# Optimization experiments

Measured on AMD Instinct MI355X. Metric: run time of the kernel, lower is better.

Reference implementation:

```python
import jax, jax.numpy as jnp
import numpy as np

NUM_NODES = 200000
NUM_EDGES = 600000
NUM_GRAPHS = 10000
BN_EPS = 1e-5


def setup_inputs() -> dict:
    key = jax.random.key(0)
    ks = jax.random.split(key, 10)
    x = jax.random.normal(ks[0], (NUM_NODES, 78), dtype=jnp.float32)
    edge_index = jax.random.randint(ks[1], (2, NUM_EDGES), 0, NUM_NODES, dtype=jnp.int64 if jax.config.jax_enable_x64 else jnp.int32)
    batch = jnp.sort(jax.random.randint(ks[2], (NUM_NODES,), 0, NUM_GRAPHS))
    def glorot(k, shape):
        fan_in, fan_out = shape[-2], shape[-1]
        s = jnp.sqrt(2.0 / (fan_in + fan_out))
        return jax.random.normal(k, shape, dtype=jnp.float32) * s
    return {
        "x": x,
        "edge_index": edge_index,
        "batch": batch,
        "W1_0": glorot(ks[3], (78, 128)),
        "b1_0": jnp.zeros((128,), jnp.float32),
        "W2_0": glorot(ks[4], (128, 128)),
        "b2_0": jnp.zeros((128,), jnp.float32),
        "g_0": jnp.ones((128,), jnp.float32),
        "be_0": jnp.zeros((128,), jnp.float32),
        "W1s": glorot(ks[5], (4, 128, 128)),
        "b1s": jnp.zeros((4, 128), jnp.float32),
        "W2s": glorot(ks[6], (4, 128, 128)),
        "b2s": jnp.zeros((4, 128), jnp.float32),
        "gs": jnp.ones((4, 128), jnp.float32),
        "bes": jnp.zeros((4, 128), jnp.float32),
        "fcW": glorot(ks[7], (128, 64)),
        "fcb": jnp.zeros((64,), jnp.float32),
    }


def _batchnorm(h, gamma, beta):
    # BatchNorm1d with batch statistics (training-mode normalization)
    mean = h.mean(axis=0)
    var = h.var(axis=0)  # biased, as torch uses for normalization
    return gamma * (h - mean) * jax.lax.rsqrt(var + BN_EPS) + beta


def _gin_block(h, src, dst, W1, b1, W2, b2, gamma, beta):
    # GINConv (eps=0): MLP(x + sum of neighbor messages), then ReLU + BN
    agg = jax.ops.segment_sum(h[src], dst, num_segments=NUM_NODES)  # [N, d]
    z = h + agg
    z = jax.nn.relu(z @ W1 + b1) @ W2 + b2
    z = jax.nn.relu(z)
    return _batchnorm(z, gamma, beta)


def reference(x, edge_index, batch, W1_0, b1_0, W2_0, b2_0, g_0, be_0,
              W1s, b1s, W2s, b2s, gs, bes, fcW, fcb):
    src, dst = edge_index[0], edge_index[1]
    h = _gin_block(x, src, dst, W1_0, b1_0, W2_0, b2_0, g_0, be_0)  # [N, 128]

    def body(h, params):
        W1, b1, W2, b2, g, be = params
        return _gin_block(h, src, dst, W1, b1, W2, b2, g, be), None

    h, _ = jax.lax.scan(body, h, (W1s, b1s, W2s, b2s, gs, bes))

    pooled = jax.ops.segment_sum(h, batch, num_segments=NUM_GRAPHS)  # [G, 128]
    out = jax.nn.relu(pooled @ fcW + fcb)  # [G, 64]; dropout is identity at eval
    return out
```

## Files before the change

### kernel.cpp

```cpp
#include <hip/hip_runtime.h>
#include <hip/hip_bf16.h>

#define NN 200000
#define NE 600000
#define NG 10000
#define NCH 98

typedef __attribute__((ext_vector_type(8))) short bfrag;
typedef __attribute__((ext_vector_type(4))) float f32x4;
typedef unsigned short u16;

static __device__ __forceinline__ u16 f2b(float x) {
  __hip_bfloat16 b = __float2bfloat16(x);
  return __builtin_bit_cast(u16, b);
}
static __device__ __forceinline__ float b2f(u16 u) {
  __hip_bfloat16 b = __builtin_bit_cast(__hip_bfloat16, u);
  return __bfloat162float(b);
}
static __device__ __forceinline__ void split(float v, u16& hi, u16& lo) {
  hi = f2b(v);
  lo = f2b(v - b2f(hi));
}

__global__ void prep_kernel(const float* __restrict__ W1_0, const float* __restrict__ W2_0,
                            const float* __restrict__ W1s, const float* __restrict__ W2s,
                            u16* __restrict__ wf) {
  int i = blockIdx.x * 256 + threadIdx.x;
  if (i >= 312 * 64) return;
  int t = i >> 6, lane = i & 63;
  const float* W;
  int KS, ct, kk, Krows, base, half;
  if (t < 24) {
    W = W1_0; KS = 3; ct = t / 3; kk = t - ct * 3; Krows = 78; base = 0; half = 12288;
  } else if (t < 56) {
    int u = t - 24;
    W = W2_0; KS = 4; ct = u >> 2; kk = u & 3; Krows = 128; base = 24576; half = 16384;
  } else {
    int u = t - 56;
    int j = u >> 6, r = u & 63;
    KS = 4; Krows = 128; half = 16384;
    if (r < 32) {
      W = W1s + j * 16384; ct = r >> 2; kk = r & 3; base = 57344 + j * 65536;
    } else {
      W = W2s + j * 16384; r -= 32; ct = r >> 2; kk = r & 3; base = 57344 + j * 65536 + 32768;
    }
  }
  int col = ct * 16 + (lane & 15);
  int idx = ((ct * KS + kk) * 64 + lane) * 8;
  for (int jj = 0; jj < 8; jj++) {
    int k = kk * 32 + 8 * (lane >> 4) + jj;
    float v = (k < Krows) ? W[k * 128 + col] : 0.f;
    u16 hi, lo;
    split(v, hi, lo);
    wf[base + idx + jj] = hi;
    wf[base + half + idx + jj] = lo;
  }
}

__global__ void hist_kernel(const int* __restrict__ dst, int* __restrict__ deg) {
  int e = blockIdx.x * 256 + threadIdx.x;
  if (e < NE) atomicAdd(&deg[dst[e]], 1);
}

__global__ void scan1_kernel(const int* __restrict__ deg, int* __restrict__ csum) {
  __shared__ int s[256];
  int base = blockIdx.x * 2048 + threadIdx.x * 8;
  int t = 0;
#pragma unroll
  for (int j = 0; j < 8; j++) {
    int idx = base + j;
    if (idx < NN) t += deg[idx];
  }
  s[threadIdx.x] = t;
  __syncthreads();
  for (int o = 128; o > 0; o >>= 1) {
    if (threadIdx.x < o) s[threadIdx.x] += s[threadIdx.x + o];
    __syncthreads();
  }
  if (threadIdx.x == 0) csum[blockIdx.x] = s[0];
}

__global__ void scan2_kernel(int* __restrict__ csum, int* __restrict__ rowptr) {
  int acc = 0;
  for (int i = 0; i < NCH; i++) {
    int v = csum[i];
    csum[i] = acc;
    acc += v;
  }
  rowptr[NN] = acc;
}

__global__ void scan3_kernel(const int* deg, const int* __restrict__ csum,
                             int* __restrict__ rowptr, int* cursor) {
  __shared__ int s[256];
  int tid = threadIdx.x;
  int base = blockIdx.x * 2048 + tid * 8;
  int loc[8];
  int t = 0;
#pragma unroll
  for (int j = 0; j < 8; j++) {
    int idx = base + j;
    int d = (idx < NN) ? deg[idx] : 0;
    loc[j] = t;
    t += d;
  }
  s[tid] = t;
  __syncthreads();
  for (int o = 1; o < 256; o <<= 1) {
    int u = (tid >= o) ? s[tid - o] : 0;
    __syncthreads();
    s[tid] += u;
    __syncthreads();
  }
  int off = csum[blockIdx.x] + s[tid] - t;
#pragma unroll
  for (int j = 0; j < 8; j++) {
    int idx = base + j;
    if (idx < NN) {
      int r = off + loc[j];
      rowptr[idx] = r;
      cursor[idx] = r;
    }
  }
}

__global__ void scatter_kernel(const int* __restrict__ src, const int* __restrict__ dst,
                               int* __restrict__ cursor, int* __restrict__ csr_src) {
  int e = blockIdx.x * 256 + threadIdx.x;
  if (e < NE) {
    int p = atomicAdd(&cursor[dst[e]], 1);
    csr_src[p] = src[e];
  }
}

template <bool FIRST>
__global__ __launch_bounds__(512, 4) void fused_kernel(
    const float* __restrict__ xin, const u16* __restrict__ hin,
    const float* __restrict__ ss,
    const int* __restrict__ rowptr, const int* __restrict__ csr_src,
    const u16* __restrict__ w1hi, const u16* __restrict__ w1lo,
    const u16* __restrict__ w2hi, const u16* __restrict__ w2lo,
    const float* __restrict__ b1, const float* __restrict__ b2,
    u16* __restrict__ hout, float* __restrict__ stats) {
  constexpr int KS1 = FIRST ? 3 : 4;
  constexpr int AH = 0, AL = 8704, TH = 17408, TL = 26112;
  __shared__ u16 lds[34816];
  const int tid = threadIdx.x;
  const int w = tid >> 6, l = tid & 63;
  const int l15 = l & 15, lg = l >> 4;
  const float bb1 = b1[w * 16 + l15];
  const float bb2 = b2[w * 16 + l15];
  float s_acc = 0.f, q_acc = 0.f;

  float sc8[8], sh8[8];
  if (!FIRST) {
    int k8 = l15 * 8;
#pragma unroll
    for (int j = 0; j < 8; j++) {
      sc8[j] = ss[k8 + j];
      sh8[j] = ss[128 + k8 + j];
    }
  }

  for (int tile = blockIdx.x; tile < 3125; tile += gridDim.x) {
    const int rows0 = tile * 64;

    if (FIRST) {
      const float2* x2 = reinterpret_cast<const float2*>(xin);
      for (int j = 0; j < 8; j++) {
        int row = w * 8 + j;
        int node = rows0 + row;
        int beg = rowptr[node], end = rowptr[node + 1];
        int f0 = l * 2;
        if (f0 < 78) {
          size_t fid = (size_t)node * 39 + (f0 >> 1);
          float2 acc = x2[fid];
          int i = beg;
          for (; i + 1 < end; i += 2) {
            int s0 = csr_src[i], s1 = csr_src[i + 1];
            float2 v0 = x2[(size_t)s0 * 39 + (f0 >> 1)];
            float2 v1 = x2[(size_t)s1 * 39 + (f0 >> 1)];
            acc.x += v0.x + v1.x;
            acc.y += v0.y + v1.y;
          }
          if (i < end) {
            int s0 = csr_src[i];
            float2 v0 = x2[(size_t)s0 * 39 + (f0 >> 1)];
            acc.x += v0.x;
            acc.y += v0.y;
          }
          ushort2 oh, ol;
          split(acc.x, oh.x, ol.x);
          split(acc.y, oh.y, ol.y);
          *reinterpret_cast<ushort2*>(&lds[AH + row * 136 + f0]) = oh;
          *reinterpret_cast<ushort2*>(&lds[AL + row * 136 + f0]) = ol;
        } else if (f0 < 96) {
          ushort2 z = {0, 0};
          *reinterpret_cast<ushort2*>(&lds[AH + row * 136 + f0]) = z;
          *reinterpret_cast<ushort2*>(&lds[AL + row * 136 + f0]) = z;
        }
      }
    } else {
      const bfrag* hp = reinterpret_cast<const bfrag*>(hin);
      const int k8v = l15;
      for (int p = 0; p < 2; p++) {
        int row = w * 8 + p * 4 + lg;
        int node = rows0 + row;
        int beg = rowptr[node], end = rowptr[node + 1];
        float a[8];
        bfrag vs = hp[(size_t)node * 16 + k8v];
#pragma unroll
        for (int j = 0; j < 8; j++) a[j] = b2f((u16)vs[j]);
        int i = beg;
        for (; i + 3 < end; i += 4) {
          int s0 = csr_src[i], s1 = csr_src[i + 1];
          int s2 = csr_src[i + 2], s3 = csr_src[i + 3];
          bfrag v0 = hp[(size_t)s0 * 16 + k8v];
          bfrag v1 = hp[(size_t)s1 * 16 + k8v];
          bfrag v2 = hp[(size_t)s2 * 16 + k8v];
          bfrag v3 = hp[(size_t)s3 * 16 + k8v];
#pragma unroll
          for (int j = 0; j < 8; j++)
            a[j] += (b2f((u16)v0[j]) + b2f((u16)v1[j])) + (b2f((u16)v2[j]) + b2f((u16)v3[j]));
        }
        for (; i < end; i++) {
          int s0 = csr_src[i];
          bfrag v0 = hp[(size_t)s0 * 16 + k8v];
#pragma unroll
          for (int j = 0; j < 8; j++) a[j] += b2f((u16)v0[j]);
        }
        float cnt = (float)(end - beg + 1);
        bfrag oh, ol;
#pragma unroll
        for (int j = 0; j < 8; j++) {
          float t = a[j] * sc8[j] + cnt * sh8[j];
          u16 hi, lo;
          split(t, hi, lo);
          oh[j] = (short)hi;
          ol[j] = (short)lo;
        }
        *reinterpret_cast<bfrag*>(&lds[AH + row * 136 + l15 * 8]) = oh;
        *reinterpret_cast<bfrag*>(&lds[AL + row * 136 + l15 * 8]) = ol;
      }
    }
    bfrag w1h[KS1], w1l[KS1];
#pragma unroll
    for (int kk = 0; kk < KS1; kk++) {
      int fi = ((w * KS1 + kk) * 64 + l) * 8;
      w1h[kk] = *reinterpret_cast<const bfrag*>(&w1hi[fi]);
      w1l[kk] = *reinterpret_cast<const bfrag*>(&w1lo[fi]);
    }
    __syncthreads();

#pragma unroll
    for (int rt = 0; rt < 4; rt++) {
      f32x4 acc = {bb1, bb1, bb1, bb1};
      const int arow = (rt * 16 + l15) * 136 + 8 * lg;
#pragma unroll
      for (int kk = 0; kk < KS1; kk++) {
        bfrag ah = *reinterpret_cast<const bfrag*>(&lds[AH + arow + kk * 32]);
        bfrag al = *reinterpret_cast<const bfrag*>(&lds[AL + arow + kk * 32]);
        acc = __builtin_amdgcn_mfma_f32_16x16x32_bf16(al, w1h[kk], acc, 0, 0, 0);
        acc = __builtin_amdgcn_mfma_f32_16x16x32_bf16(ah, w1l[kk], acc, 0, 0, 0);
        acc = __builtin_amdgcn_mfma_f32_16x16x32_bf16(ah, w1h[kk], acc, 0, 0, 0);
      }
#pragma unroll
      for (int r = 0; r < 4; r++) {
        float v = fmaxf(acc[r], 0.f);
        u16 hi, lo;
        split(v, hi, lo);
        int off = (rt * 16 + 4 * lg + r) * 136 + w * 16 + l15;
        lds[TH + off] = hi;
        lds[TL + off] = lo;
      }
    }
    bfrag w2h[4], w2l[4];
#pragma unroll
    for (int kk = 0; kk < 4; kk++) {
      int fi = ((w * 4 + kk) * 64 + l) * 8;
      w2h[kk] = *reinterpret_cast<const bfrag*>(&w2hi[fi]);
      w2l[kk] = *reinterpret_cast<const bfrag*>(&w2lo[fi]);
    }
    __syncthreads();

#pragma unroll
    for (int rt = 0; rt < 4; rt++) {
      f32x4 acc = {bb2, bb2, bb2, bb2};
      const int arow = (rt * 16 + l15) * 136 + 8 * lg;
#pragma unroll
      for (int kk = 0; kk < 4; kk++) {
        bfrag th = *reinterpret_cast<const bfrag*>(&lds[TH + arow + kk * 32]);
        bfrag tl = *reinterpret_cast<const bfrag*>(&lds[TL + arow + kk * 32]);
        acc = __builtin_amdgcn_mfma_f32_16x16x32_bf16(tl, w2h[kk], acc, 0, 0, 0);
        acc = __builtin_amdgcn_mfma_f32_16x16x32_bf16(th, w2l[kk], acc, 0, 0, 0);
        acc = __builtin_amdgcn_mfma_f32_16x16x32_bf16(th, w2h[kk], acc, 0, 0, 0);
      }
#pragma unroll
      for (int r = 0; r < 4; r++) {
        float v = fmaxf(acc[r], 0.f);
        hout[(size_t)(rows0 + rt * 16 + 4 * lg + r) * 128 + w * 16 + l15] = f2b(v);
        s_acc += v;
        q_acc += v * v;
      }
    }
    __syncthreads();
  }
  s_acc += __shfl_xor(s_acc, 16);
  s_acc += __shfl_xor(s_acc, 32);
  q_acc += __shfl_xor(q_acc, 16);
  q_acc += __shfl_xor(q_acc, 32);
  if (lg == 0) {
    atomicAdd(&stats[w * 16 + l15], s_acc);
    atomicAdd(&stats[128 + w * 16 + l15], q_acc);
  }
}

__global__ void bn_kernel(const float* __restrict__ stats, const float* __restrict__ gamma,
                          const float* __restrict__ beta, float* __restrict__ ss) {
  int c = threadIdx.x;
  float mean = stats[c] * (1.f / NN);
  float var = stats[128 + c] * (1.f / NN) - mean * mean;
  var = fmaxf(var, 0.f);
  float sc = gamma[c] * rsqrtf(var + 1e-5f);
  ss[c] = sc;
  ss[128 + c] = beta[c] - mean * sc;
}

__global__ void pool_kernel(const u16* __restrict__ h, const float* __restrict__ ss,
                            const int* __restrict__ batch, float* __restrict__ pooled) {
  int c = threadIdx.x;
  int n0 = blockIdx.x * 128;
  int n1 = min(n0 + 128, NN);
  float sc = ss[c], sh = ss[128 + c];
  float acc = 0.f;
  float cnt = 0.f;
  int gprev = batch[n0];
  for (int n = n0; n < n1; n++) {
    int g = batch[n];
    if (g != gprev) {
      atomicAdd(&pooled[gprev * 128 + c], sc * acc + cnt * sh);
      acc = 0.f;
      cnt = 0.f;
      gprev = g;
    }
    acc += b2f(h[(size_t)n * 128 + c]);
    cnt += 1.f;
  }
  atomicAdd(&pooled[gprev * 128 + c], sc * acc + cnt * sh);
}

__global__ void fc_kernel(const float* __restrict__ pooled, const float* __restrict__ fcW,
                          const float* __restrict__ fcb, float* __restrict__ out) {
  int i = blockIdx.x * 256 + threadIdx.x;
  if (i >= NG * 64) return;
  int g = i >> 6, o = i & 63;
  float acc = fcb[o];
#pragma unroll 8
  for (int k = 0; k < 128; k++) acc += pooled[g * 128 + k] * fcW[k * 64 + o];
  out[i] = fmaxf(acc, 0.f);
}

extern "C" void kernel_launch(void* const* d_in, const int* in_sizes, int n_in,
                              void* d_out, int out_size, void* d_ws, size_t ws_size,
                              hipStream_t stream) {
  const float* x = (const float*)d_in[0];
  const int* ei = (const int*)d_in[1];
  const int* src = ei;
  const int* dst = ei + NE;
  const int* batch = (const int*)d_in[2];
  const float* W1_0 = (const float*)d_in[3];
  const float* b1_0 = (const float*)d_in[4];
  const float* W2_0 = (const float*)d_in[5];
  const float* b2_0 = (const float*)d_in[6];
  const float* g_0 = (const float*)d_in[7];
  const float* be_0 = (const float*)d_in[8];
  const float* W1s = (const float*)d_in[9];
  const float* b1s = (const float*)d_in[10];
  const float* W2s = (const float*)d_in[11];
  const float* b2s = (const float*)d_in[12];
  const float* gs = (const float*)d_in[13];
  const float* bes = (const float*)d_in[14];
  const float* fcW = (const float*)d_in[15];
  const float* fcb = (const float*)d_in[16];

  char* ws = (char*)d_ws;
  u16* buf0 = (u16*)(ws + 0);
  u16* buf1 = (u16*)(ws + 51200000);
  float* POOLED = (float*)(ws + 102400000);
  float* STATS = (float*)(ws + 107520000);
  float* SS = (float*)(ws + 107521024);
  u16* WF = (u16*)(ws + 107522048);
  int* ROWPTR = (int*)(ws + 108161024);
  int* CURSOR = (int*)(ws + 108961040);
  int* CSRC = (int*)(ws + 109761040);
  int* CSUM = (int*)(ws + 112161040);

  prep_kernel<<<78, 256, 0, stream>>>(W1_0, W2_0, W1s, W2s, WF);

  hipMemsetAsync(CURSOR, 0, NN * 4, stream);
  hist_kernel<<<(NE + 255) / 256, 256, 0, stream>>>(dst, CURSOR);
  scan1_kernel<<<NCH, 256, 0, stream>>>(CURSOR, CSUM);
  scan2_kernel<<<1, 1, 0, stream>>>(CSUM, ROWPTR);
  scan3_kernel<<<NCH, 256, 0, stream>>>(CURSOR, CSUM, ROWPTR, CURSOR);
  scatter_kernel<<<(NE + 255) / 256, 256, 0, stream>>>(src, dst, CURSOR, CSRC);

  u16* buf[2] = {buf0, buf1};
  hipMemsetAsync(STATS, 0, 1024, stream);
  fused_kernel<true><<<512, 512, 0, stream>>>(x, nullptr, nullptr, ROWPTR, CSRC,
                                              WF, WF + 12288, WF + 24576, WF + 40960,
                                              b1_0, b2_0, buf0, STATS);
  bn_kernel<<<1, 128, 0, stream>>>(STATS, g_0, be_0, SS);

  for (int L = 1; L < 5; L++) {
    int j = L - 1;
    const u16* hin = buf[(L + 1) & 1];
    u16* hb = buf[L & 1];
    hipMemsetAsync(STATS, 0, 1024, stream);
    const u16* wl = WF + 57344 + j * 65536;
    fused_kernel<false><<<512, 512, 0, stream>>>(nullptr, hin, SS, ROWPTR, CSRC,
                                                 wl, wl + 16384, wl + 32768, wl + 49152,
                                                 b1s + j * 128, b2s + j * 128, hb, STATS);
    bn_kernel<<<1, 128, 0, stream>>>(STATS, gs + j * 128, bes + j * 128, SS);
  }

  hipMemsetAsync(POOLED, 0, (size_t)NG * 128 * 4, stream);
  pool_kernel<<<(NN + 127) / 128, 128, 0, stream>>>(buf[0], SS, batch, POOLED);
  fc_kernel<<<(NG * 64 + 255) / 256, 256, 0, stream>>>(POOLED, fcW, fcb, (float*)d_out);
}
```

Baseline: 690.9 us.

## Halve fused-kernel row tile to raise occupancy and branchless neighbor gathers

```diff
diff --git a/kernel.cpp b/kernel.cpp
--- a/kernel.cpp
+++ b/kernel.cpp
@@ -5,6 +5,7 @@
 #define NE 600000
 #define NG 10000
 #define NCH 98
+#define NTILE 6250
 
 typedef __attribute__((ext_vector_type(8))) short bfrag;
 typedef __attribute__((ext_vector_type(4))) float f32x4;
@@ -135,7 +136,7 @@
 }
 
 template <bool FIRST>
-__global__ __launch_bounds__(512, 4) void fused_kernel(
+__global__ __launch_bounds__(512, 8) void fused_kernel(
     const float* __restrict__ xin, const u16* __restrict__ hin,
     const float* __restrict__ ss,
     const int* __restrict__ rowptr, const int* __restrict__ csr_src,
@@ -144,8 +145,8 @@
     const float* __restrict__ b1, const float* __restrict__ b2,
     u16* __restrict__ hout, float* __restrict__ stats) {
   constexpr int KS1 = FIRST ? 3 : 4;
-  constexpr int AH = 0, AL = 8704, TH = 17408, TL = 26112;
-  __shared__ u16 lds[34816];
+  constexpr int AH = 0, AL = 4352, TH = 8704, TL = 13056;
+  __shared__ u16 lds[17408];
   const int tid = threadIdx.x;
   const int w = tid >> 6, l = tid & 63;
   const int l15 = l & 15, lg = l >> 4;
@@ -153,42 +154,31 @@
   const float bb2 = b2[w * 16 + l15];
   float s_acc = 0.f, q_acc = 0.f;
 
-  float sc8[8], sh8[8];
-  if (!FIRST) {
-    int k8 = l15 * 8;
-#pragma unroll
-    for (int j = 0; j < 8; j++) {
-      sc8[j] = ss[k8 + j];
-      sh8[j] = ss[128 + k8 + j];
-    }
-  }
-
-  for (int tile = blockIdx.x; tile < 3125; tile += gridDim.x) {
-    const int rows0 = tile * 64;
+  for (int tile = blockIdx.x; tile < NTILE; tile += gridDim.x) {
+    const int rows0 = tile * 32;
 
     if (FIRST) {
       const float2* x2 = reinterpret_cast<const float2*>(xin);
-      for (int j = 0; j < 8; j++) {
-        int row = w * 8 + j;
+      for (int j = 0; j < 4; j++) {
+        int row = w * 4 + j;
         int node = rows0 + row;
         int beg = rowptr[node], end = rowptr[node + 1];
         int f0 = l * 2;
         if (f0 < 78) {
-          size_t fid = (size_t)node * 39 + (f0 >> 1);
-          float2 acc = x2[fid];
-          int i = beg;
-          for (; i + 1 < end; i += 2) {
-            int s0 = csr_src[i], s1 = csr_src[i + 1];
-            float2 v0 = x2[(size_t)s0 * 39 + (f0 >> 1)];
-            float2 v1 = x2[(size_t)s1 * 39 + (f0 >> 1)];
-            acc.x += v0.x + v1.x;
-            acc.y += v0.y + v1.y;
-          }
-          if (i < end) {
-            int s0 = csr_src[i];
-            float2 v0 = x2[(size_t)s0 * 39 + (f0 >> 1)];
-            acc.x += v0.x;
-            acc.y += v0.y;
+          size_t fv = (size_t)(f0 >> 1);
+          float2 acc = x2[(size_t)node * 39 + fv];
+          for (int i = beg; i < end; i += 4) {
+            int last = end - 1;
+            int i1 = min(i + 1, last), i2 = min(i + 2, last), i3 = min(i + 3, last);
+            int s0 = csr_src[i], s1 = csr_src[i1], s2 = csr_src[i2], s3 = csr_src[i3];
+            float2 v0 = x2[(size_t)s0 * 39 + fv];
+            float2 v1 = x2[(size_t)s1 * 39 + fv];
+            float2 v2 = x2[(size_t)s2 * 39 + fv];
+            float2 v3 = x2[(size_t)s3 * 39 + fv];
+            int rem = end - i;
+            float m1 = rem > 1 ? 1.f : 0.f, m2 = rem > 2 ? 1.f : 0.f, m3 = rem > 3 ? 1.f : 0.f;
+            acc.x += v0.x + m1 * v1.x + m2 * v2.x + m3 * v3.x;
+            acc.y += v0.y + m1 * v1.y + m2 * v2.y + m3 * v3.y;
           }
           ushort2 oh, ol;
           split(acc.x, oh.x, ol.x);
@@ -204,45 +194,48 @@
     } else {
       const bfrag* hp = reinterpret_cast<const bfrag*>(hin);
       const int k8v = l15;
-      for (int p = 0; p < 2; p++) {
-        int row = w * 8 + p * 4 + lg;
-        int node = rows0 + row;
-        int beg = rowptr[node], end = rowptr[node + 1];
-        float a[8];
-        bfrag vs = hp[(size_t)node * 16 + k8v];
-#pragma unroll
-        for (int j = 0; j < 8; j++) a[j] = b2f((u16)vs[j]);
-        int i = beg;
-        for (; i + 3 < end; i += 4) {
-          int s0 = csr_src[i], s1 = csr_src[i + 1];
-          int s2 = csr_src[i + 2], s3 = csr_src[i + 3];
-          bfrag v0 = hp[(size_t)s0 * 16 + k8v];
-          bfrag v1 = hp[(size_t)s1 * 16 + k8v];
-          bfrag v2 = hp[(size_t)s2 * 16 + k8v];
-          bfrag v3 = hp[(size_t)s3 * 16 + k8v];
-#pragma unroll
-          for (int j = 0; j < 8; j++)
-            a[j] += (b2f((u16)v0[j]) + b2f((u16)v1[j])) + (b2f((u16)v2[j]) + b2f((u16)v3[j]));
-        }
-        for (; i < end; i++) {
-          int s0 = csr_src[i];
-          bfrag v0 = hp[(size_t)s0 * 16 + k8v];
-#pragma unroll
-          for (int j = 0; j < 8; j++) a[j] += b2f((u16)v0[j]);
-        }
-        float cnt = (float)(end - beg + 1);
-        bfrag oh, ol;
-#pragma unroll
-        for (int j = 0; j < 8; j++) {
-          float t = a[j] * sc8[j] + cnt * sh8[j];
-          u16 hi, lo;
-          split(t, hi, lo);
-          oh[j] = (short)hi;
-          ol[j] = (short)lo;
-        }
-        *reinterpret_cast<bfrag*>(&lds[AH + row * 136 + l15 * 8]) = oh;
-        *reinterpret_cast<bfrag*>(&lds[AL + row * 136 + l15 * 8]) = ol;
-      }
+      int k8 = l15 * 8;
+      float4 scA = *reinterpret_cast<const float4*>(&ss[k8]);
+      float4 scB = *reinterpret_cast<const float4*>(&ss[k8 + 4]);
+      float4 shA = *reinterpret_cast<const float4*>(&ss[128 + k8]);
+      float4 shB = *reinterpret_cast<const float4*>(&ss[128 + k8 + 4]);
+      float sc8[8] = {scA.x, scA.y, scA.z, scA.w, scB.x, scB.y, scB.z, scB.w};
+      float sh8[8] = {shA.x, shA.y, shA.z, shA.w, shB.x, shB.y, shB.z, shB.w};
+
+      int row = w * 4 + lg;
+      int node = rows0 + row;
+      int beg = rowptr[node], end = rowptr[node + 1];
+      float a[8];
+      bfrag vs = hp[(size_t)node * 16 + k8v];
+#pragma unroll
+      for (int j = 0; j < 8; j++) a[j] = b2f((u16)vs[j]);
+      for (int i = beg; i < end; i += 4) {
+        int last = end - 1;
+        int i1 = min(i + 1, last), i2 = min(i + 2, last), i3 = min(i + 3, last);
+        int s0 = csr_src[i], s1 = csr_src[i1], s2 = csr_src[i2], s3 = csr_src[i3];
+        bfrag v0 = hp[(size_t)s0 * 16 + k8v];
+        bfrag v1 = hp[(size_t)s1 * 16 + k8v];
+        bfrag v2 = hp[(size_t)s2 * 16 + k8v];
+        bfrag v3 = hp[(size_t)s3 * 16 + k8v];
+        int rem = end - i;
+        float m1 = rem > 1 ? 1.f : 0.f, m2 = rem > 2 ? 1.f : 0.f, m3 = rem > 3 ? 1.f : 0.f;
+#pragma unroll
+        for (int j = 0; j < 8; j++)
+          a[j] += (b2f((u16)v0[j]) + m1 * b2f((u16)v1[j])) +
+                  (m2 * b2f((u16)v2[j]) + m3 * b2f((u16)v3[j]));
+      }
+      float cnt = (float)(end - beg + 1);
+      bfrag oh, ol;
+#pragma unroll
+      for (int j = 0; j < 8; j++) {
+        float t = a[j] * sc8[j] + cnt * sh8[j];
+        u16 hi, lo;
+        split(t, hi, lo);
+        oh[j] = (short)hi;
+        ol[j] = (short)lo;
+      }
+      *reinterpret_cast<bfrag*>(&lds[AH + row * 136 + k8]) = oh;
+      *reinterpret_cast<bfrag*>(&lds[AL + row * 136 + k8]) = ol;
     }
     bfrag w1h[KS1], w1l[KS1];
 #pragma unroll
@@ -254,7 +247,7 @@
     __syncthreads();
 
 #pragma unroll
-    for (int rt = 0; rt < 4; rt++) {
+    for (int rt = 0; rt < 2; rt++) {
       f32x4 acc = {bb1, bb1, bb1, bb1};
       const int arow = (rt * 16 + l15) * 136 + 8 * lg;
 #pragma unroll
@@ -285,7 +278,7 @@
     __syncthreads();
 
 #pragma unroll
-    for (int rt = 0; rt < 4; rt++) {
+    for (int rt = 0; rt < 2; rt++) {
       f32x4 acc = {bb2, bb2, bb2, bb2};
       const int arow = (rt * 16 + l15) * 136 + 8 * lg;
 #pragma unroll
@@ -407,9 +400,9 @@
 
   u16* buf[2] = {buf0, buf1};
   hipMemsetAsync(STATS, 0, 1024, stream);
-  fused_kernel<true><<<512, 512, 0, stream>>>(x, nullptr, nullptr, ROWPTR, CSRC,
-                                              WF, WF + 12288, WF + 24576, WF + 40960,
-                                              b1_0, b2_0, buf0, STATS);
+  fused_kernel<true><<<1024, 512, 0, stream>>>(x, nullptr, nullptr, ROWPTR, CSRC,
+                                               WF, WF + 12288, WF + 24576, WF + 40960,
+                                               b1_0, b2_0, buf0, STATS);
   bn_kernel<<<1, 128, 0, stream>>>(STATS, g_0, be_0, SS);
 
   for (int L = 1; L < 5; L++) {
@@ -418,9 +411,9 @@
     u16* hb = buf[L & 1];
     hipMemsetAsync(STATS, 0, 1024, stream);
     const u16* wl = WF + 57344 + j * 65536;
-    fused_kernel<false><<<512, 512, 0, stream>>>(nullptr, hin, SS, ROWPTR, CSRC,
-                                                 wl, wl + 16384, wl + 32768, wl + 49152,
-                                                 b1s + j * 128, b2s + j * 128, hb, STATS);
+    fused_kernel<false><<<1024, 512, 0, stream>>>(nullptr, hin, SS, ROWPTR, CSRC,
+                                                  wl, wl + 16384, wl + 32768, wl + 49152,
+                                                  b1s + j * 128, b2s + j * 128, hb, STATS);
     bn_kernel<<<1, 128, 0, stream>>>(STATS, gs + j * 128, bes + j * 128, SS);
   }
 
```

After: 1.337 ms. 1.93x slower.

## Halve LDS footprint by reusing one buffer and stage coalesced output stores

Applied to the files above, without the earlier changes.

```diff
diff --git a/kernel.cpp b/kernel.cpp
--- a/kernel.cpp
+++ b/kernel.cpp
@@ -5,6 +5,7 @@
 #define NE 600000
 #define NG 10000
 #define NCH 98
+#define NTILE 3125
 
 typedef __attribute__((ext_vector_type(8))) short bfrag;
 typedef __attribute__((ext_vector_type(4))) float f32x4;
@@ -135,7 +136,7 @@
 }
 
 template <bool FIRST>
-__global__ __launch_bounds__(512, 4) void fused_kernel(
+__global__ __launch_bounds__(512, 6) void fused_kernel(
     const float* __restrict__ xin, const u16* __restrict__ hin,
     const float* __restrict__ ss,
     const int* __restrict__ rowptr, const int* __restrict__ csr_src,
@@ -144,8 +145,8 @@
     const float* __restrict__ b1, const float* __restrict__ b2,
     u16* __restrict__ hout, float* __restrict__ stats) {
   constexpr int KS1 = FIRST ? 3 : 4;
-  constexpr int AH = 0, AL = 8704, TH = 17408, TL = 26112;
-  __shared__ u16 lds[34816];
+  constexpr int XH = 0, XL = 8704;
+  __shared__ u16 lds[17408];
   const int tid = threadIdx.x;
   const int w = tid >> 6, l = tid & 63;
   const int l15 = l & 15, lg = l >> 4;
@@ -163,7 +164,7 @@
     }
   }
 
-  for (int tile = blockIdx.x; tile < 3125; tile += gridDim.x) {
+  for (int tile = blockIdx.x; tile < NTILE; tile += gridDim.x) {
     const int rows0 = tile * 64;
 
     if (FIRST) {
@@ -174,31 +175,31 @@
         int beg = rowptr[node], end = rowptr[node + 1];
         int f0 = l * 2;
         if (f0 < 78) {
-          size_t fid = (size_t)node * 39 + (f0 >> 1);
-          float2 acc = x2[fid];
+          size_t fv = (size_t)(f0 >> 1);
+          float2 acc = x2[(size_t)node * 39 + fv];
           int i = beg;
           for (; i + 1 < end; i += 2) {
             int s0 = csr_src[i], s1 = csr_src[i + 1];
-            float2 v0 = x2[(size_t)s0 * 39 + (f0 >> 1)];
-            float2 v1 = x2[(size_t)s1 * 39 + (f0 >> 1)];
+            float2 v0 = x2[(size_t)s0 * 39 + fv];
+            float2 v1 = x2[(size_t)s1 * 39 + fv];
             acc.x += v0.x + v1.x;
             acc.y += v0.y + v1.y;
           }
           if (i < end) {
             int s0 = csr_src[i];
-            float2 v0 = x2[(size_t)s0 * 39 + (f0 >> 1)];
+            float2 v0 = x2[(size_t)s0 * 39 + fv];
             acc.x += v0.x;
             acc.y += v0.y;
           }
           ushort2 oh, ol;
           split(acc.x, oh.x, ol.x);
           split(acc.y, oh.y, ol.y);
-          *reinterpret_cast<ushort2*>(&lds[AH + row * 136 + f0]) = oh;
-          *reinterpret_cast<ushort2*>(&lds[AL + row * 136 + f0]) = ol;
+          *reinterpret_cast<ushort2*>(&lds[XH + row * 136 + f0]) = oh;
+          *reinterpret_cast<ushort2*>(&lds[XL + row * 136 + f0]) = ol;
         } else if (f0 < 96) {
           ushort2 z = {0, 0};
-          *reinterpret_cast<ushort2*>(&lds[AH + row * 136 + f0]) = z;
-          *reinterpret_cast<ushort2*>(&lds[AL + row * 136 + f0]) = z;
+          *reinterpret_cast<ushort2*>(&lds[XH + row * 136 + f0]) = z;
+          *reinterpret_cast<ushort2*>(&lds[XL + row * 136 + f0]) = z;
         }
       }
     } else {
@@ -240,8 +241,8 @@
           oh[j] = (short)hi;
           ol[j] = (short)lo;
         }
-        *reinterpret_cast<bfrag*>(&lds[AH + row * 136 + l15 * 8]) = oh;
-        *reinterpret_cast<bfrag*>(&lds[AL + row * 136 + l15 * 8]) = ol;
+        *reinterpret_cast<bfrag*>(&lds[XH + row * 136 + l15 * 8]) = oh;
+        *reinterpret_cast<bfrag*>(&lds[XL + row * 136 + l15 * 8]) = ol;
       }
     }
     bfrag w1h[KS1], w1l[KS1];
@@ -253,26 +254,33 @@
     }
     __syncthreads();
 
+    f32x4 t1[4];
 #pragma unroll
     for (int rt = 0; rt < 4; rt++) {
       f32x4 acc = {bb1, bb1, bb1, bb1};
       const int arow = (rt * 16 + l15) * 136 + 8 * lg;
 #pragma unroll
       for (int kk = 0; kk < KS1; kk++) {
-        bfrag ah = *reinterpret_cast<const bfrag*>(&lds[AH + arow + kk * 32]);
-        bfrag al = *reinterpret_cast<const bfrag*>(&lds[AL + arow + kk * 32]);
+        bfrag ah = *reinterpret_cast<const bfrag*>(&lds[XH + arow + kk * 32]);
+        bfrag al = *reinterpret_cast<const bfrag*>(&lds[XL + arow + kk * 32]);
         acc = __builtin_amdgcn_mfma_f32_16x16x32_bf16(al, w1h[kk], acc, 0, 0, 0);
         acc = __builtin_amdgcn_mfma_f32_16x16x32_bf16(ah, w1l[kk], acc, 0, 0, 0);
         acc = __builtin_amdgcn_mfma_f32_16x16x32_bf16(ah, w1h[kk], acc, 0, 0, 0);
       }
+      t1[rt] = acc;
+    }
+    __syncthreads();
+
+#pragma unroll
+    for (int rt = 0; rt < 4; rt++) {
 #pragma unroll
       for (int r = 0; r < 4; r++) {
-        float v = fmaxf(acc[r], 0.f);
+        float v = fmaxf(t1[rt][r], 0.f);
         u16 hi, lo;
         split(v, hi, lo);
         int off = (rt * 16 + 4 * lg + r) * 136 + w * 16 + l15;
-        lds[TH + off] = hi;
-        lds[TL + off] = lo;
+        lds[XH + off] = hi;
+        lds[XL + off] = lo;
       }
     }
     bfrag w2h[4], w2l[4];
@@ -284,14 +292,15 @@
     }
     __syncthreads();
 
+    u16 o16[16];
 #pragma unroll
     for (int rt = 0; rt < 4; rt++) {
       f32x4 acc = {bb2, bb2, bb2, bb2};
       const int arow = (rt * 16 + l15) * 136 + 8 * lg;
 #pragma unroll
       for (int kk = 0; kk < 4; kk++) {
-        bfrag th = *reinterpret_cast<const bfrag*>(&lds[TH + arow + kk * 32]);
-        bfrag tl = *reinterpret_cast<const bfrag*>(&lds[TL + arow + kk * 32]);
+        bfrag th = *reinterpret_cast<const bfrag*>(&lds[XH + arow + kk * 32]);
+        bfrag tl = *reinterpret_cast<const bfrag*>(&lds[XL + arow + kk * 32]);
         acc = __builtin_amdgcn_mfma_f32_16x16x32_bf16(tl, w2h[kk], acc, 0, 0, 0);
         acc = __builtin_amdgcn_mfma_f32_16x16x32_bf16(th, w2l[kk], acc, 0, 0, 0);
         acc = __builtin_amdgcn_mfma_f32_16x16x32_bf16(th, w2h[kk], acc, 0, 0, 0);
@@ -299,10 +308,28 @@
 #pragma unroll
       for (int r = 0; r < 4; r++) {
         float v = fmaxf(acc[r], 0.f);
-        hout[(size_t)(rows0 + rt * 16 + 4 * lg + r) * 128 + w * 16 + l15] = f2b(v);
         s_acc += v;
         q_acc += v * v;
-      }
+        o16[rt * 4 + r] = f2b(v);
+      }
+    }
+    __syncthreads();
+
+#pragma unroll
+    for (int rt = 0; rt < 4; rt++) {
+#pragma unroll
+      for (int r = 0; r < 4; r++) {
+        lds[XH + (rt * 16 + 4 * lg + r) * 136 + w * 16 + l15] = o16[rt * 4 + r];
+      }
+    }
+    __syncthreads();
+
+#pragma unroll
+    for (int p = 0; p < 2; p++) {
+      int row = p * 32 + (tid >> 4);
+      int c8 = tid & 15;
+      bfrag vv = *reinterpret_cast<const bfrag*>(&lds[XH + row * 136 + c8 * 8]);
+      *reinterpret_cast<bfrag*>(&hout[(size_t)(rows0 + row) * 128 + c8 * 8]) = vv;
     }
     __syncthreads();
   }
@@ -407,7 +434,7 @@
 
   u16* buf[2] = {buf0, buf1};
   hipMemsetAsync(STATS, 0, 1024, stream);
-  fused_kernel<true><<<512, 512, 0, stream>>>(x, nullptr, nullptr, ROWPTR, CSRC,
+  fused_kernel<true><<<768, 512, 0, stream>>>(x, nullptr, nullptr, ROWPTR, CSRC,
                                               WF, WF + 12288, WF + 24576, WF + 40960,
                                               b1_0, b2_0, buf0, STATS);
   bn_kernel<<<1, 128, 0, stream>>>(STATS, g_0, be_0, SS);
@@ -418,7 +445,7 @@
     u16* hb = buf[L & 1];
     hipMemsetAsync(STATS, 0, 1024, stream);
     const u16* wl = WF + 57344 + j * 65536;
-    fused_kernel<false><<<512, 512, 0, stream>>>(nullptr, hin, SS, ROWPTR, CSRC,
+    fused_kernel<false><<<768, 512, 0, stream>>>(nullptr, hin, SS, ROWPTR, CSRC,
                                                  wl, wl + 16384, wl + 32768, wl + 49152,
                                                  b1s + j * 128, b2s + j * 128, hb, STATS);
     bn_kernel<<<1, 128, 0, stream>>>(STATS, gs + j * 128, bes + j * 128, SS);
```

Result: slower. 882.5 us (+27.7%).
